# Optimization experiments

Hardware: AMD Instinct MI355X
Metric: run time of the kernel (lower is better)

Reference implementation:

```python
import jax, jax.numpy as jnp
import numpy as np

N_INPUT, NUM_CENTERS, DIM = 16384, 4096, 256


def setup_inputs() -> dict:
    key = jax.random.key(0)
    k1, k2, k3, k4 = jax.random.split(key, 4)
    x = jax.random.normal(k1, (N_INPUT, DIM), dtype=jnp.float32)
    centers = jax.random.normal(k2, (NUM_CENTERS, DIM), dtype=jnp.float32)
    # positive sigmas bounded away from 0 so exp(-d^2/2s^2) stays well-scaled
    sigmas = jax.random.uniform(k3, (NUM_CENTERS, DIM), dtype=jnp.float32) * 2.0 + 1.0
    w_lin = jax.random.normal(k4, (1, NUM_CENTERS), dtype=jnp.float32) * (1.0 / np.sqrt(NUM_CENTERS))
    b_lin = jnp.zeros((1,), dtype=jnp.float32)
    return {"x": x, "centers": centers, "sigmas": sigmas, "w_lin": w_lin, "b_lin": b_lin}


def reference(x, centers, sigmas, w_lin, b_lin):
    # Anisotropic squared Mahalanobis-style distance:
    #   d2[n,c] = sum_d (x[n,d]-centers[c,d])^2 / (2*sigmas[c,d]^2)
    # expanded into GEMMs to avoid the (n, c, d) intermediate.
    inv2s2 = 1.0 / (2.0 * sigmas * sigmas)                      # [C, D]
    d2 = (
        jnp.einsum("nd,cd->nc", x * x, inv2s2)                 # x^2 term
        - 2.0 * jnp.einsum("nd,cd->nc", x, centers * inv2s2)   # cross term
        + jnp.sum(centers * centers * inv2s2, axis=-1)          # c^2 term [C]
    )
    radial_val = jnp.exp(-d2)                                   # [N, C]
    class_score = radial_val @ w_lin.T + b_lin                  # [N, 1]
    return jax.nn.sigmoid(class_score)
```

## Files before the change

kernel.cpp:

```cpp
#include <hip/hip_runtime.h>
#include <cstdint>
#include <cstddef>

#define MDIM 16384
#define CDIM 4096
#define DDIM 256
#define KDIM 512
#define KB   256

typedef float f32x4  __attribute__((ext_vector_type(4)));
typedef float f32x16 __attribute__((ext_vector_type(16)));
typedef int   i32x4v __attribute__((ext_vector_type(4)));
typedef int   i32x8v __attribute__((ext_vector_type(8)));

__device__ __forceinline__ unsigned q4(float v) {
    unsigned s = (__builtin_bit_cast(unsigned, v) >> 31) << 3;
    float a = fabsf(v);
    unsigned c = (unsigned)(a >= 0.25f) + (a >= 0.75f) + (a >= 1.25f)
               + (a >= 1.75f) + (a >= 2.5f) + (a >= 3.5f) + (a >= 5.0f);
    return s | c;
}
__device__ __forceinline__ unsigned pack8(const float* v) {
    unsigned w = 0;
    #pragma unroll
    for (int i = 0; i < 8; ++i) w |= q4(v[i]) << (4 * i);
    return w;
}

__global__ __launch_bounds__(256) void prep(
    const float* __restrict__ x, const float* __restrict__ centers,
    const float* __restrict__ sigmas,
    unsigned char* __restrict__ Ap, unsigned char* __restrict__ Bp,
    float* __restrict__ constc, float* __restrict__ score) {
    int b = blockIdx.x, tid = threadIdx.x;
    if (b < 2048) {
        int idx8 = b * 256 + tid;
        int n = idx8 >> 5, d8 = idx8 & 31;
        float v[8], v2[8];
        *(float4*)(v)     = ((const float4*)x)[idx8 * 2];
        *(float4*)(v + 4) = ((const float4*)x)[idx8 * 2 + 1];
        #pragma unroll
        for (int i = 0; i < 8; ++i) v2[i] = v[i] * v[i] * 0.125f;
        *(unsigned*)(Ap + (size_t)n * KB + d8 * 4)       = pack8(v);
        *(unsigned*)(Ap + (size_t)n * KB + 128 + d8 * 4) = pack8(v2);
        if (idx8 < MDIM) score[idx8] = 0.0f;
    } else {
        int gid8 = (b - 2048) * 256 + tid;
        int c = gid8 >> 5, d8 = gid8 & 31;
        float cv[8], sv[8], cr[8], iv[8];
        *(float4*)(cv)     = ((const float4*)centers)[gid8 * 2];
        *(float4*)(cv + 4) = ((const float4*)centers)[gid8 * 2 + 1];
        *(float4*)(sv)     = ((const float4*)sigmas)[gid8 * 2];
        *(float4*)(sv + 4) = ((const float4*)sigmas)[gid8 * 2 + 1];
        float t = 0.0f;
        #pragma unroll
        for (int i = 0; i < 8; ++i) {
            float inv = 1.0f / (2.0f * sv[i] * sv[i]);
            cr[i] = -2.0f * cv[i] * inv;
            iv[i] = inv * 8.0f;
            t += cv[i] * cv[i] * inv;
        }
        *(unsigned*)(Bp + (size_t)c * KB + d8 * 4)       = pack8(cr);
        *(unsigned*)(Bp + (size_t)c * KB + 128 + d8 * 4) = pack8(iv);
        #pragma unroll
        for (int m = 16; m; m >>= 1) t += __shfl_xor(t, m, 64);
        if ((tid & 31) == 0) constc[c] = t;
    }
}

__global__ __launch_bounds__(256, 3) void gemm_fused(
    const unsigned char* __restrict__ A, const unsigned char* __restrict__ B,
    const float* __restrict__ constc, const float* __restrict__ w,
    float* __restrict__ score) {

    __shared__ unsigned char As[128 * 128];
    __shared__ unsigned char Bs[128 * 128];

    const int tid  = threadIdx.x;
    const int wave = tid >> 6;
    const int lane = tid & 63;
    const int l32  = lane & 31;
    const int half = lane >> 5;

    const int bm = blockIdx.y;
    const int bn = blockIdx.x;

    const int wave_m = wave * 32;

    f32x16 acc[4] = {};

    const float NEG_LOG2E = -1.4426950408889634f;
    float wj4[4], cjl4[4];
    #pragma unroll
    for (int j = 0; j < 4; ++j) {
        int ng = bn * 128 + j * 32 + l32;
        wj4[j]  = w[ng];
        cjl4[j] = NEG_LOG2E * constc[ng];
    }

    const int st_row = lane >> 3;
    const int st_k   = ((lane & 7) ^ st_row) * 16;

    const unsigned char* Abase = A + (size_t)(bm * 128) * KB;
    const unsigned char* Bbase = B + (size_t)(bn * 128) * KB;

    const int rsw = l32 & 7;

    #pragma unroll
    for (int k0 = 0; k0 < 2; ++k0) {
        const int sA = k0 ? 0x82828282 : 0x7F7F7F7F;
        const int sB = k0 ? 0x7C7C7C7C : 0x7F7F7F7F;
        #pragma unroll
        for (int c = 0; c < 4; ++c) {
            int slab = wave * 4 + c;
            const unsigned char* ga = Abase + (size_t)(slab * 8 + st_row) * KB + k0 * 128 + st_k;
            __builtin_amdgcn_global_load_lds(
                (const __attribute__((address_space(1))) void*)ga,
                (__attribute__((address_space(3))) void*)(As + slab * 1024), 16, 0, 0);
        }
        #pragma unroll
        for (int c = 0; c < 4; ++c) {
            int slab = wave * 4 + c;
            const unsigned char* gb = Bbase + (size_t)(slab * 8 + st_row) * KB + k0 * 128 + st_k;
            __builtin_amdgcn_global_load_lds(
                (const __attribute__((address_space(1))) void*)gb,
                (__attribute__((address_space(3))) void*)(Bs + slab * 1024), 16, 0, 0);
        }
        __syncthreads();

        #pragma unroll
        for (int s = 0; s < 4; ++s) {
            const int sl = ((2 * s + half) ^ rsw) * 16;
            i32x4v alo = *(const i32x4v*)(As + (wave_m + l32) * 128 + sl);
            i32x8v af  = __builtin_shufflevector(alo, alo, 0, 1, 2, 3, -1, -1, -1, -1);
            #pragma unroll
            for (int j = 0; j < 4; ++j) {
                i32x4v blo = *(const i32x4v*)(Bs + (j * 32 + l32) * 128 + sl);
                i32x8v bf  = __builtin_shufflevector(blo, blo, 0, 1, 2, 3, -1, -1, -1, -1);
                acc[j] = __builtin_amdgcn_mfma_scale_f32_32x32x64_f8f6f4(
                    af, bf, acc[j],
                    4 , 4 ,
                    0, sA, 0, sB);
            }
        }
        __syncthreads();
    }

    float rowsum[16];
    #pragma unroll
    for (int r = 0; r < 16; ++r) rowsum[r] = 0.0f;

    #pragma unroll
    for (int j = 0; j < 4; ++j) {
        float wj  = wj4[j];
        float cjl = cjl4[j];
        #pragma unroll
        for (int r = 0; r < 16; ++r)
            rowsum[r] += exp2f(fmaf(acc[j][r], NEG_LOG2E, cjl)) * wj;
    }

    #pragma unroll
    for (int mask = 1; mask < 32; mask <<= 1)
        #pragma unroll
        for (int r = 0; r < 16; ++r)
            rowsum[r] += __shfl_xor(rowsum[r], mask, 64);

    if (l32 == 0) {
        #pragma unroll
        for (int r = 0; r < 16; ++r) {
            int mg = bm * 128 + wave_m + (r & 3) + 8 * (r >> 2) + 4 * half;
            atomicAdd(&score[mg], rowsum[r]);
        }
    }
}

__global__ void finalize(const float* __restrict__ score,
                         const float* __restrict__ b,
                         float* __restrict__ out) {
    int n = blockIdx.x * 256 + threadIdx.x;
    if (n < MDIM) {
        float s = score[n] + b[0];
        out[n] = 1.0f / (1.0f + exp2f(-1.4426950408889634f * s));
    }
}

extern "C" void kernel_launch(void* const* d_in, const int* in_sizes, int n_in,
                              void* d_out, int out_size, void* d_ws, size_t ws_size,
                              hipStream_t stream) {
    const float* x       = (const float*)d_in[0];
    const float* centers = (const float*)d_in[1];
    const float* sigmas  = (const float*)d_in[2];
    const float* w_lin   = (const float*)d_in[3];
    const float* b_lin   = (const float*)d_in[4];
    float* out = (float*)d_out;

    char* ws = (char*)d_ws;
    unsigned char* Ap = (unsigned char*)ws;
    unsigned char* Bp = (unsigned char*)(ws + (size_t)MDIM * KB);
    float* cc    = (float*)(ws + (size_t)MDIM * KB + (size_t)CDIM * KB);
    float* score = (float*)((char*)cc + CDIM * sizeof(float));

    prep<<<dim3(2048 + 512), dim3(256), 0, stream>>>(
        x, centers, sigmas, Ap, Bp, cc, score);
    gemm_fused<<<dim3(CDIM / 128, MDIM / 128), dim3(256), 0, stream>>>(
        Ap, Bp, cc, w_lin, score);
    finalize<<<dim3((MDIM + 255) / 256), dim3(256), 0, stream>>>(score, b_lin, out);
}
```

Baseline: 131.0 us.

## Reuse B tile across two M blocks and switch to 16x16x128 scaled MFMA

Each workgroup now keeps the full 128-column B tile (both K halves) resident in LDS and processes two 128-row A blocks in sequence, halving the grid and B global traffic. The MFMA shape changes from 32x32x64 to 16x16x128, with accumulators reorganised as 2x8 f32x4 and the epilogue reduction shortened to 16-lane shuffles. The epilogue for the first M block is overlapped with staging of the next A tile. In exchange, LDS use rises to 48KB per block, which may reduce occupancy against the launch bound of 3 blocks.

```diff
diff --git a/kernel.cpp b/kernel.cpp
--- a/kernel.cpp
+++ b/kernel.cpp
@@ -9,7 +9,6 @@
 #define KB   256
 
 typedef float f32x4  __attribute__((ext_vector_type(4)));
-typedef float f32x16 __attribute__((ext_vector_type(16)));
 typedef int   i32x4v __attribute__((ext_vector_type(4)));
 typedef int   i32x8v __attribute__((ext_vector_type(8)));
 
@@ -73,105 +72,147 @@
     const float* __restrict__ constc, const float* __restrict__ w,
     float* __restrict__ score) {
 
+    __shared__ unsigned char Bs[2 * 128 * 128];
     __shared__ unsigned char As[128 * 128];
-    __shared__ unsigned char Bs[128 * 128];
 
     const int tid  = threadIdx.x;
     const int wave = tid >> 6;
     const int lane = tid & 63;
-    const int l32  = lane & 31;
-    const int half = lane >> 5;
-
-    const int bm = blockIdx.y;
-    const int bn = blockIdx.x;
+    const int quad = lane >> 4;
+    const int l16  = lane & 15;
+
+    const int bn  = blockIdx.x;
+    const int bm0 = blockIdx.y * 2;
 
     const int wave_m = wave * 32;
 
-    f32x16 acc[4] = {};
-
     const float NEG_LOG2E = -1.4426950408889634f;
-    float wj4[4], cjl4[4];
-    #pragma unroll
-    for (int j = 0; j < 4; ++j) {
-        int ng = bn * 128 + j * 32 + l32;
-        wj4[j]  = w[ng];
-        cjl4[j] = NEG_LOG2E * constc[ng];
-    }
 
     const int st_row = lane >> 3;
     const int st_k   = ((lane & 7) ^ st_row) * 16;
 
-    const unsigned char* Abase = A + (size_t)(bm * 128) * KB;
     const unsigned char* Bbase = B + (size_t)(bn * 128) * KB;
-
-    const int rsw = l32 & 7;
+    const unsigned char* A0    = A + (size_t)(bm0 * 128) * KB;
+    const unsigned char* A1    = A0 + (size_t)128 * KB;
+
+    const int rsw = l16 & 7;
+
+    f32x4 acc[2][8] = {};
+
+    #define STAGE_A(abase, k0)                                                     \
+        {                                                                          \
+            _Pragma("unroll")                                                      \
+            for (int c = 0; c < 4; ++c) {                                          \
+                int slab = wave * 4 + c;                                           \
+                const unsigned char* ga =                                          \
+                    (abase) + (size_t)(slab * 8 + st_row) * KB + (k0) * 128 + st_k;\
+                __builtin_amdgcn_global_load_lds(                                  \
+                    (const __attribute__((address_space(1))) void*)ga,             \
+                    (__attribute__((address_space(3))) void*)(As + slab * 1024),   \
+                    16, 0, 0);                                                     \
+            }                                                                      \
+        }
+
+    #define COMPUTE(k0)                                                            \
+        {                                                                          \
+            const int sA = (k0) ? 0x82828282 : 0x7F7F7F7F;                         \
+            const int sB = (k0) ? 0x7C7C7C7C : 0x7F7F7F7F;                         \
+            const unsigned char* bs = Bs + (k0) * 16384;                           \
+            _Pragma("unroll")                                                      \
+            for (int kh = 0; kh < 2; ++kh) {                                       \
+                const int sl = ((kh * 4 + quad) ^ rsw) * 16;                       \
+                i32x8v af[2];                                                      \
+                _Pragma("unroll")                                                  \
+                for (int i = 0; i < 2; ++i) {                                      \
+                    i32x4v lo = *(const i32x4v*)(As + (wave_m + i * 16 + l16) * 128 + sl); \
+                    af[i] = __builtin_shufflevector(lo, lo, 0, 1, 2, 3, -1, -1, -1, -1);   \
+                }                                                                  \
+                _Pragma("unroll")                                                  \
+                for (int j = 0; j < 8; ++j) {                                      \
+                    i32x4v lo = *(const i32x4v*)(bs + (j * 16 + l16) * 128 + sl);  \
+                    i32x8v bf = __builtin_shufflevector(lo, lo, 0, 1, 2, 3, -1, -1, -1, -1); \
+                    _Pragma("unroll")                                              \
+                    for (int i = 0; i < 2; ++i)                                    \
+                        acc[i][j] = __builtin_amdgcn_mfma_scale_f32_16x16x128_f8f6f4( \
+                            af[i], bf, acc[i][j], 4, 4, 0, sA, 0, sB);             \
+                }                                                                  \
+            }                                                                      \
+        }
+
+    #define EPILOGUE(bmrow)                                                        \
+        {                                                                          \
+            float rowsum[2][4];                                                    \
+            _Pragma("unroll")                                                      \
+            for (int i = 0; i < 2; ++i)                                            \
+                _Pragma("unroll")                                                  \
+                for (int r = 0; r < 4; ++r) rowsum[i][r] = 0.0f;                   \
+            _Pragma("unroll")                                                      \
+            for (int j = 0; j < 8; ++j) {                                          \
+                int ng = bn * 128 + j * 16 + l16;                                  \
+                float wj  = w[ng];                                                 \
+                float cjl = NEG_LOG2E * constc[ng];                                \
+                _Pragma("unroll")                                                  \
+                for (int i = 0; i < 2; ++i)                                        \
+                    _Pragma("unroll")                                              \
+                    for (int r = 0; r < 4; ++r)                                    \
+                        rowsum[i][r] += exp2f(fmaf(acc[i][j][r], NEG_LOG2E, cjl)) * wj; \
+            }                                                                      \
+            _Pragma("unroll")                                                      \
+            for (int mask = 1; mask < 16; mask <<= 1)                              \
+                _Pragma("unroll")                                                  \
+                for (int i = 0; i < 2; ++i)                                        \
+                    _Pragma("unroll")                                              \
+                    for (int r = 0; r < 4; ++r)                                    \
+                        rowsum[i][r] += __shfl_xor(rowsum[i][r], mask, 64);        \
+            if (l16 == 0) {                                                        \
+                _Pragma("unroll")                                                  \
+                for (int i = 0; i < 2; ++i)                                        \
+                    _Pragma("unroll")                                              \
+                    for (int r = 0; r < 4; ++r) {                                  \
+                        int mg = (bmrow) * 128 + wave_m + i * 16 + quad * 4 + r;   \
+                        atomicAdd(&score[mg], rowsum[i][r]);                       \
+                    }                                                              \
+            }                                                                      \
+            _Pragma("unroll")                                                      \
+            for (int i = 0; i < 2; ++i)                                            \
+                _Pragma("unroll")                                                  \
+                for (int j = 0; j < 8; ++j) acc[i][j] = (f32x4){0,0,0,0};          \
+        }
 
     #pragma unroll
     for (int k0 = 0; k0 < 2; ++k0) {
-        const int sA = k0 ? 0x82828282 : 0x7F7F7F7F;
-        const int sB = k0 ? 0x7C7C7C7C : 0x7F7F7F7F;
-        #pragma unroll
-        for (int c = 0; c < 4; ++c) {
-            int slab = wave * 4 + c;
-            const unsigned char* ga = Abase + (size_t)(slab * 8 + st_row) * KB + k0 * 128 + st_k;
-            __builtin_amdgcn_global_load_lds(
-                (const __attribute__((address_space(1))) void*)ga,
-                (__attribute__((address_space(3))) void*)(As + slab * 1024), 16, 0, 0);
-        }
         #pragma unroll
         for (int c = 0; c < 4; ++c) {
             int slab = wave * 4 + c;
             const unsigned char* gb = Bbase + (size_t)(slab * 8 + st_row) * KB + k0 * 128 + st_k;
             __builtin_amdgcn_global_load_lds(
                 (const __attribute__((address_space(1))) void*)gb,
-                (__attribute__((address_space(3))) void*)(Bs + slab * 1024), 16, 0, 0);
-        }
-        __syncthreads();
-
-        #pragma unroll
-        for (int s = 0; s < 4; ++s) {
-            const int sl = ((2 * s + half) ^ rsw) * 16;
-            i32x4v alo = *(const i32x4v*)(As + (wave_m + l32) * 128 + sl);
-            i32x8v af  = __builtin_shufflevector(alo, alo, 0, 1, 2, 3, -1, -1, -1, -1);
-            #pragma unroll
-            for (int j = 0; j < 4; ++j) {
-                i32x4v blo = *(const i32x4v*)(Bs + (j * 32 + l32) * 128 + sl);
-                i32x8v bf  = __builtin_shufflevector(blo, blo, 0, 1, 2, 3, -1, -1, -1, -1);
-                acc[j] = __builtin_amdgcn_mfma_scale_f32_32x32x64_f8f6f4(
-                    af, bf, acc[j],
-                    4 , 4 ,
-                    0, sA, 0, sB);
-            }
-        }
-        __syncthreads();
+                (__attribute__((address_space(3))) void*)(Bs + k0 * 16384 + slab * 1024),
+                16, 0, 0);
+        }
     }
-
-    float rowsum[16];
-    #pragma unroll
-    for (int r = 0; r < 16; ++r) rowsum[r] = 0.0f;
-
-    #pragma unroll
-    for (int j = 0; j < 4; ++j) {
-        float wj  = wj4[j];
-        float cjl = cjl4[j];
-        #pragma unroll
-        for (int r = 0; r < 16; ++r)
-            rowsum[r] += exp2f(fmaf(acc[j][r], NEG_LOG2E, cjl)) * wj;
-    }
-
-    #pragma unroll
-    for (int mask = 1; mask < 32; mask <<= 1)
-        #pragma unroll
-        for (int r = 0; r < 16; ++r)
-            rowsum[r] += __shfl_xor(rowsum[r], mask, 64);
-
-    if (l32 == 0) {
-        #pragma unroll
-        for (int r = 0; r < 16; ++r) {
-            int mg = bm * 128 + wave_m + (r & 3) + 8 * (r >> 2) + 4 * half;
-            atomicAdd(&score[mg], rowsum[r]);
-        }
-    }
+    STAGE_A(A0, 0);
+    __syncthreads();
+
+    COMPUTE(0);
+    __syncthreads();
+    STAGE_A(A0, 1);
+    __syncthreads();
+    COMPUTE(1);
+    __syncthreads();
+    STAGE_A(A1, 0);
+    EPILOGUE(bm0);
+    __syncthreads();
+    COMPUTE(0);
+    __syncthreads();
+    STAGE_A(A1, 1);
+    __syncthreads();
+    COMPUTE(1);
+    EPILOGUE(bm0 + 1);
+
+    #undef STAGE_A
+    #undef COMPUTE
+    #undef EPILOGUE
 }
 
 __global__ void finalize(const float* __restrict__ score,
@@ -202,7 +243,7 @@
 
     prep<<<dim3(2048 + 512), dim3(256), 0, stream>>>(
         x, centers, sigmas, Ap, Bp, cc, score);
-    gemm_fused<<<dim3(CDIM / 128, MDIM / 128), dim3(256), 0, stream>>>(
+    gemm_fused<<<dim3(CDIM / 128, MDIM / 256), dim3(256), 0, stream>>>(
         Ap, Bp, cc, w_lin, score);
     finalize<<<dim3((MDIM + 255) / 256), dim3(256), 0, stream>>>(score, b_lin, out);
 }
```

Measured after the change: 120.2 us. -8.2%, faster.
